# Optimization experiments

Hardware: AMD Instinct MI355X
Metric: run time of the kernel (lower is better)

The kernel has to match this reference:

```python
import jax, jax.numpy as jnp
import numpy as np


def _phi(z, conv_w, conv_b):
    # z: (H, W, S, 1) -> 3x3 SAME conv over state channels -> softmax over states
    x = jnp.transpose(z[..., 0], (2, 0, 1))[None]  # (1, S, H, W)
    y = jax.lax.conv_general_dilated(
        x, conv_w, window_strides=(1, 1), padding='SAME',
        dimension_numbers=('NCHW', 'OIHW', 'NCHW')) + conv_b[None, :, None, None]
    return jax.nn.softmax(jnp.transpose(y[0], (1, 2, 0)), axis=2)[..., None]  # (H, W, S, 1)


def _update(obs, P, u_k, w_k_O, conv_w, conv_b):
    H, W, O = obs.shape
    S = P.shape[0]
    # b = P^T @ obs per cell: b[h,w,s] = sum_o P[o,s] * obs[h,w,o]
    b = jnp.einsum('os,hwo->hws', P, obs)[..., None]  # (H, W, S, 1)
    # Analytic Jacobian db/dP: deriv_b[h,w,s,0,i,j] = obs[h,w,i] * delta(s==j)
    eye = jnp.eye(S, O, dtype=obs.dtype)
    deriv_b = (obs[:, :, None, :, None] * eye[None, None, :, None, :])[:, :, :, None, :, :]  # (H,W,S,1,S,O)

    Bu = b * u_k                                  # (H, W, S, 1)
    bu = jnp.sum(Bu, axis=2, keepdims=True)       # (H, W, 1, 1)
    Z = Bu / bu                                   # Bu / bu

    u_kp1 = _phi(Z, conv_w, conv_b)               # (H, W, S, 1)

    # Sensitivity recursion for obs params (quotient rule on Bu/bu)
    du = deriv_b * u_k[..., None, None] + b[..., None, None] * w_k_O  # (H,W,S,1,S,O)
    term1 = du * bu[..., None, None]
    term2 = jnp.expand_dims(jnp.sum(du, axis=2), 3) * Bu[..., None, None]
    w_pre = (term1 - term2) / bu[..., None, None] ** 2                # (H,W,S,1,S,O)

    # J @ w  ==  9 JVPs of Phi at Z with tangent columns of w (exact, avoids dense (HWS)^2 Jacobian)
    tangents = jnp.moveaxis(w_pre.reshape(H, W, S, 1, S * O), -1, 0)  # (S*O, H, W, S, 1)
    jvp1 = lambda t: jax.jvp(lambda z: _phi(z, conv_w, conv_b), (Z,), (t,))[1]
    w_kp1_O = jnp.moveaxis(jax.vmap(jvp1)(tangents), 0, -1).reshape(H, W, S, 1, S, O)
    return u_kp1, w_kp1_O


def setup_inputs() -> dict:
    key = jax.random.key(0)
    k1, k2, k3 = jax.random.split(key, 3)
    H = W = 512
    S = O = 3
    obs = jax.random.uniform(k1, (H, W, O), dtype=jnp.float32)
    obs_param_matrix = jnp.ones((S, O), jnp.float32) / O          # row-stochastic init
    u_k = jnp.ones((H, W, S, 1), jnp.float32) / S                 # uniform belief
    w_k_O = jnp.zeros((H, W, S, 1, S, O), jnp.float32)
    conv_w = jax.random.normal(k2, (S, S, 3, 3), jnp.float32) * 0.1
    conv_b = jax.random.normal(k3, (S,), jnp.float32) * 0.1
    return {'obs': obs, 'obs_param_matrix': obs_param_matrix, 'u_k': u_k,
            'w_k_O': w_k_O, 'conv_w': conv_w, 'conv_b': conv_b}


def reference(obs, obs_param_matrix, u_k, w_k_O, conv_w, conv_b):
    return _update(obs, obs_param_matrix, u_k, w_k_O, conv_w, conv_b)
```

## Files before the change

kernel.cpp:

```cpp
#include <hip/hip_runtime.h>

#define IMH 512
#define IMW 512
#define TW 32
#define TH 8
#define HW_ (TW + 2)
#define HH_ (TH + 2)
#define NHALO (HW_ * HH_)
#define NTHR 256

__global__ __launch_bounds__(NTHR, 2)
void hmm_fused(const float* __restrict__ obs,
               const float* __restrict__ P,
               const float* __restrict__ u_k,
               const float* __restrict__ w_k,
               const float* __restrict__ conv_w,
               const float* __restrict__ conv_b,
               float* __restrict__ out) {
    __shared__ float4 lds4[NHALO * 8];
    float* lds = (float*)lds4;

    const int tid = threadIdx.x;
    const int w0 = blockIdx.x * TW;
    const int h0 = blockIdx.y * TH;

    float Pm[9];
#pragma unroll
    for (int i = 0; i < 9; ++i) Pm[i] = P[i];

    for (int r = 0; r < HH_; ++r) {
        const int hh = h0 + r - 1;
        if (hh < 0 || hh >= IMH) continue;
        const long long gbase = ((long long)hh * IMW + (w0 - 1)) * 27;
        for (int f = tid; f < HW_ * 27; f += NTHR) {
            const int p = f / 27;
            const int c = f - p * 27;
            const int ww = w0 - 1 + p;
            float v = 0.0f;
            if (ww >= 0 && ww < IMW) v = w_k[gbase + f];
            const int pr = r * HW_ + p;
            lds[pr * 32 + (((c >> 2) + pr) & 7) * 4 + (c & 3)] = v;
        }
    }

    float cw[81];
#pragma unroll
    for (int i = 0; i < 81; ++i) cw[i] = conv_w[i];
    const float cb0 = conv_b[0], cb1 = conv_b[1], cb2 = conv_b[2];

    __syncthreads();

    for (int p = tid; p < NHALO; p += NTHR) {
        const int rr = p / HW_;
        const int cc = p - rr * HW_;
        const int hh = h0 + rr - 1;
        const int ww = w0 + cc - 1;
        float4 o[8];
        if ((unsigned)hh < IMH && (unsigned)ww < IMW) {
            float wv[28];
#pragma unroll
            for (int k = 0; k < 7; ++k) {
                const float4 v = lds4[p * 8 + ((k + p) & 7)];
                wv[4 * k + 0] = v.x; wv[4 * k + 1] = v.y;
                wv[4 * k + 2] = v.z; wv[4 * k + 3] = v.w;
            }
            const int pix = hh * IMW + ww;
            const float ov0 = obs[pix * 3 + 0], ov1 = obs[pix * 3 + 1], ov2 = obs[pix * 3 + 2];
            const float us[3] = {u_k[pix * 3 + 0], u_k[pix * 3 + 1], u_k[pix * 3 + 2]};

            float b[3], Bu[3], bu = 0.0f;
#pragma unroll
            for (int s = 0; s < 3; ++s) {
                b[s] = Pm[0 * 3 + s] * ov0 + Pm[1 * 3 + s] * ov1 + Pm[2 * 3 + s] * ov2;
                Bu[s] = b[s] * us[s];
                bu += Bu[s];
            }
            const float inv_bu = 1.0f / bu;
            float Z[3], oc[32];
#pragma unroll
            for (int s = 0; s < 3; ++s) { Z[s] = Bu[s] * inv_bu; oc[s] = Z[s]; }

            const float ovv[3] = {ov0, ov1, ov2};
#pragma unroll
            for (int i = 0; i < 3; ++i) {
#pragma unroll
                for (int j = 0; j < 3; ++j) {
                    const int ij = i * 3 + j;
                    float du[3], sdu = 0.0f;
#pragma unroll
                    for (int s = 0; s < 3; ++s) {
                        float d = b[s] * wv[s * 9 + ij];
                        if (s == j) d += ovv[i] * us[s];
                        du[s] = d;
                        sdu += d;
                    }
#pragma unroll
                    for (int s = 0; s < 3; ++s)
                        oc[3 + ij * 3 + s] = (du[s] - sdu * Z[s]) * inv_bu;
                }
            }
            oc[30] = 0.0f; oc[31] = 0.0f;
#pragma unroll
            for (int k = 0; k < 8; ++k)
                o[k] = make_float4(oc[4 * k + 0], oc[4 * k + 1], oc[4 * k + 2], oc[4 * k + 3]);
        } else {
#pragma unroll
            for (int k = 0; k < 8; ++k) o[k] = make_float4(0.f, 0.f, 0.f, 0.f);
        }
#pragma unroll
        for (int k = 0; k < 8; ++k) lds4[p * 8 + ((k + p) & 7)] = o[k];
    }

    __syncthreads();

    const int tx = tid & (TW - 1);
    const int ty = tid >> 5;
    const int hp = (ty + 1) * HW_ + tx + 1;

    float acc[30];
#pragma unroll
    for (int i = 0; i < 30; ++i) acc[i] = 0.0f;

#pragma unroll
    for (int ky = 0; ky < 3; ++ky) {
#pragma unroll
        for (int kx = 0; kx < 3; ++kx) {
            const int tap = ky * 3 + kx;
            const int pn = hp + (ky - 1) * HW_ + (kx - 1);
#pragma unroll
            for (int k = 0; k < 8; ++k) {
                const float4 v4 = lds4[pn * 8 + ((k + pn) & 7)];
                const float cv[4] = {v4.x, v4.y, v4.z, v4.w};
#pragma unroll
                for (int j = 0; j < 4; ++j) {
                    const int c = 4 * k + j;
                    if (c < 30) {
                        const int g = c / 3, si = c - (c / 3) * 3;
                        acc[g * 3 + 0] += cw[0 * 27 + si * 9 + tap] * cv[j];
                        acc[g * 3 + 1] += cw[1 * 27 + si * 9 + tap] * cv[j];
                        acc[g * 3 + 2] += cw[2 * 27 + si * 9 + tap] * cv[j];
                    }
                }
            }
        }
    }

    const float y0 = acc[0] + cb0, y1 = acc[1] + cb1, y2 = acc[2] + cb2;
    const float m = fmaxf(y0, fmaxf(y1, y2));
    const float e0 = __expf(y0 - m), e1 = __expf(y1 - m), e2 = __expf(y2 - m);
    const float inv = 1.0f / (e0 + e1 + e2);
    const float p0 = e0 * inv, p1 = e1 * inv, p2 = e2 * inv;

    const int pix = (h0 + ty) * IMW + (w0 + tx);
    out[pix * 3 + 0] = p0; out[pix * 3 + 1] = p1; out[pix * 3 + 2] = p2;

    float wout[27];
#pragma unroll
    for (int g = 1; g < 10; ++g) {
        const float a0 = acc[g * 3 + 0], a1 = acc[g * 3 + 1], a2 = acc[g * 3 + 2];
        const float dot = p0 * a0 + p1 * a1 + p2 * a2;
        const int ij = g - 1;
        wout[0 * 9 + ij] = p0 * (a0 - dot);
        wout[1 * 9 + ij] = p1 * (a1 - dot);
        wout[2 * 9 + ij] = p2 * (a2 - dot);
    }

    __syncthreads();

#pragma unroll
    for (int c = 0; c < 27; ++c) lds[tid * 27 + c] = wout[c];
    __syncthreads();

    float* outw = out + IMH * IMW * 3;
    for (int idx = tid; idx < TW * TH * 27 / 4; idx += NTHR) {
        const int r = idx / 216;
        const int q = idx - r * 216;
        const float4 v = lds4[r * 216 + q];
        float4* dst = (float4*)(outw + ((size_t)(h0 + r) * IMW + w0) * 27);
        dst[q] = v;
    }
}

extern "C" void kernel_launch(void* const* d_in, const int* in_sizes, int n_in,
                              void* d_out, int out_size, void* d_ws, size_t ws_size,
                              hipStream_t stream) {
    const float* obs    = (const float*)d_in[0];
    const float* P      = (const float*)d_in[1];
    const float* u_k    = (const float*)d_in[2];
    const float* w_k    = (const float*)d_in[3];
    const float* conv_w = (const float*)d_in[4];
    const float* conv_b = (const float*)d_in[5];
    float* out = (float*)d_out;

    dim3 grid(IMW / TW, IMH / TH);
    hmm_fused<<<grid, NTHR, 0, stream>>>(obs, P, u_k, w_k, conv_w, conv_b, out);
}
```

Measured before the change: 127.3 us.

## Split sensitivity channels across wave pairs with 512-thread blocks

```diff
diff --git a/kernel.cpp b/kernel.cpp
--- a/kernel.cpp
+++ b/kernel.cpp
@@ -4,12 +4,12 @@
 #define IMW 512
 #define TW 32
 #define TH 8
-#define HW_ (TW + 2)
-#define HH_ (TH + 2)
-#define NHALO (HW_ * HH_)
-#define NTHR 256
-
-__global__ __launch_bounds__(NTHR, 2)
+#define HW_ 34
+#define HH_ 10
+#define NHALO 340
+#define NTHR 512
+
+__global__ __launch_bounds__(NTHR, 1)
 void hmm_fused(const float* __restrict__ obs,
                const float* __restrict__ P,
                const float* __restrict__ u_k,
@@ -20,9 +20,13 @@
     __shared__ float4 lds4[NHALO * 8];
     float* lds = (float*)lds4;
 
-    const int tid = threadIdx.x;
-    const int w0 = blockIdx.x * TW;
-    const int h0 = blockIdx.y * TH;
+    const int tid  = threadIdx.x;
+    const int w0   = blockIdx.x * TW;
+    const int h0   = blockIdx.y * TH;
+    const int lane = tid & 63;
+    const int wave = tid >> 6;
+    const int q    = wave & 1;
+    const int grp  = wave >> 1;
 
     float Pm[9];
 #pragma unroll
@@ -38,8 +42,11 @@
             const int ww = w0 - 1 + p;
             float v = 0.0f;
             if (ww >= 0 && ww < IMW) v = w_k[gbase + f];
+            const int s  = c / 9;
+            const int ij = c - s * 9;
+            const int cd = (ij < 4) ? (3 + ij * 3 + s) : (16 + (ij - 4) * 3 + s);
             const int pr = r * HW_ + p;
-            lds[pr * 32 + (((c >> 2) + pr) & 7) * 4 + (c & 3)] = v;
+            lds[pr * 32 + (((cd >> 2) + pr) & 7) * 4 + (cd & 3)] = v;
         }
     }
 
@@ -50,134 +57,202 @@
 
     __syncthreads();
 
-    for (int p = tid; p < NHALO; p += NTHR) {
+    for (int p = grp * 64 + lane; p < NHALO; p += 256) {
         const int rr = p / HW_;
         const int cc = p - rr * HW_;
         const int hh = h0 + rr - 1;
         const int ww = w0 + cc - 1;
-        float4 o[8];
+        const int base = p * 8;
+        const int kb = q * 4;
+        float oc[16];
         if ((unsigned)hh < IMH && (unsigned)ww < IMW) {
-            float wv[28];
-#pragma unroll
-            for (int k = 0; k < 7; ++k) {
-                const float4 v = lds4[p * 8 + ((k + p) & 7)];
-                wv[4 * k + 0] = v.x; wv[4 * k + 1] = v.y;
-                wv[4 * k + 2] = v.z; wv[4 * k + 3] = v.w;
-            }
             const int pix = hh * IMW + ww;
-            const float ov0 = obs[pix * 3 + 0], ov1 = obs[pix * 3 + 1], ov2 = obs[pix * 3 + 2];
-            const float us[3] = {u_k[pix * 3 + 0], u_k[pix * 3 + 1], u_k[pix * 3 + 2]};
-
-            float b[3], Bu[3], bu = 0.0f;
+            const float ov[3] = {obs[pix*3+0], obs[pix*3+1], obs[pix*3+2]};
+            const float us[3] = {u_k[pix*3+0], u_k[pix*3+1], u_k[pix*3+2]};
+            float b[3], Bu[3], bu = 0.f;
 #pragma unroll
             for (int s = 0; s < 3; ++s) {
-                b[s] = Pm[0 * 3 + s] * ov0 + Pm[1 * 3 + s] * ov1 + Pm[2 * 3 + s] * ov2;
-                Bu[s] = b[s] * us[s];
-                bu += Bu[s];
+                b[s] = Pm[s] * ov[0] + Pm[3+s] * ov[1] + Pm[6+s] * ov[2];
+                Bu[s] = b[s] * us[s]; bu += Bu[s];
             }
             const float inv_bu = 1.0f / bu;
-            float Z[3], oc[32];
-#pragma unroll
-            for (int s = 0; s < 3; ++s) { Z[s] = Bu[s] * inv_bu; oc[s] = Z[s]; }
-
-            const float ovv[3] = {ov0, ov1, ov2};
-#pragma unroll
-            for (int i = 0; i < 3; ++i) {
-#pragma unroll
-                for (int j = 0; j < 3; ++j) {
-                    const int ij = i * 3 + j;
-                    float du[3], sdu = 0.0f;
+            float Z[3];
+#pragma unroll
+            for (int s = 0; s < 3; ++s) Z[s] = Bu[s] * inv_bu;
+
+            float rv[16];
+#pragma unroll
+            for (int k = 0; k < 4; ++k) {
+                const float4 v = lds4[base + ((kb + k + p) & 7)];
+                rv[4*k+0] = v.x; rv[4*k+1] = v.y; rv[4*k+2] = v.z; rv[4*k+3] = v.w;
+            }
+            if (q == 0) {
+                oc[0] = Z[0]; oc[1] = Z[1]; oc[2] = Z[2];
+#pragma unroll
+                for (int ij = 0; ij < 4; ++ij) {
+                    const int i = ij / 3, j = ij % 3;
+                    float du[3], sdu = 0.f;
 #pragma unroll
                     for (int s = 0; s < 3; ++s) {
-                        float d = b[s] * wv[s * 9 + ij];
-                        if (s == j) d += ovv[i] * us[s];
-                        du[s] = d;
-                        sdu += d;
+                        float d = b[s] * rv[3 + ij*3 + s];
+                        if (s == j) d += ov[i] * us[s];
+                        du[s] = d; sdu += d;
                     }
 #pragma unroll
                     for (int s = 0; s < 3; ++s)
-                        oc[3 + ij * 3 + s] = (du[s] - sdu * Z[s]) * inv_bu;
-                }
-            }
-            oc[30] = 0.0f; oc[31] = 0.0f;
-#pragma unroll
-            for (int k = 0; k < 8; ++k)
-                o[k] = make_float4(oc[4 * k + 0], oc[4 * k + 1], oc[4 * k + 2], oc[4 * k + 3]);
+                        oc[3 + ij*3 + s] = (du[s] - sdu * Z[s]) * inv_bu;
+                }
+                oc[15] = 0.f;
+            } else {
+#pragma unroll
+                for (int ij = 4; ij < 9; ++ij) {
+                    const int i = ij / 3, j = ij % 3;
+                    float du[3], sdu = 0.f;
+#pragma unroll
+                    for (int s = 0; s < 3; ++s) {
+                        float d = b[s] * rv[(ij-4)*3 + s];
+                        if (s == j) d += ov[i] * us[s];
+                        du[s] = d; sdu += d;
+                    }
+#pragma unroll
+                    for (int s = 0; s < 3; ++s)
+                        oc[(ij-4)*3 + s] = (du[s] - sdu * Z[s]) * inv_bu;
+                }
+                oc[15] = 0.f;
+            }
         } else {
 #pragma unroll
-            for (int k = 0; k < 8; ++k) o[k] = make_float4(0.f, 0.f, 0.f, 0.f);
-        }
-#pragma unroll
-        for (int k = 0; k < 8; ++k) lds4[p * 8 + ((k + p) & 7)] = o[k];
-    }
-
-    __syncthreads();
-
-    const int tx = tid & (TW - 1);
-    const int ty = tid >> 5;
+            for (int i = 0; i < 16; ++i) oc[i] = 0.f;
+        }
+#pragma unroll
+        for (int k = 0; k < 4; ++k)
+            lds4[base + ((kb + k + p) & 7)] =
+                make_float4(oc[4*k], oc[4*k+1], oc[4*k+2], oc[4*k+3]);
+    }
+
+    __syncthreads();
+
+    const int pxi = grp * 64 + lane;
+    const int tx = pxi & 31, ty = pxi >> 5;
     const int hp = (ty + 1) * HW_ + tx + 1;
 
-    float acc[30];
-#pragma unroll
-    for (int i = 0; i < 30; ++i) acc[i] = 0.0f;
-
-#pragma unroll
-    for (int ky = 0; ky < 3; ++ky) {
-#pragma unroll
-        for (int kx = 0; kx < 3; ++kx) {
-            const int tap = ky * 3 + kx;
-            const int pn = hp + (ky - 1) * HW_ + (kx - 1);
-#pragma unroll
-            for (int k = 0; k < 8; ++k) {
-                const float4 v4 = lds4[pn * 8 + ((k + pn) & 7)];
-                const float cv[4] = {v4.x, v4.y, v4.z, v4.w};
-#pragma unroll
-                for (int j = 0; j < 4; ++j) {
-                    const int c = 4 * k + j;
-                    if (c < 30) {
-                        const int g = c / 3, si = c - (c / 3) * 3;
-                        acc[g * 3 + 0] += cw[0 * 27 + si * 9 + tap] * cv[j];
-                        acc[g * 3 + 1] += cw[1 * 27 + si * 9 + tap] * cv[j];
-                        acc[g * 3 + 2] += cw[2 * 27 + si * 9 + tap] * cv[j];
-                    }
-                }
-            }
-        }
-    }
-
-    const float y0 = acc[0] + cb0, y1 = acc[1] + cb1, y2 = acc[2] + cb2;
-    const float m = fmaxf(y0, fmaxf(y1, y2));
-    const float e0 = __expf(y0 - m), e1 = __expf(y1 - m), e2 = __expf(y2 - m);
+    float yv0 = cb0, yv1 = cb1, yv2 = cb2;
+    float acc[15];
+#pragma unroll
+    for (int i = 0; i < 15; ++i) acc[i] = 0.f;
+
+    if (q == 0) {
+#pragma unroll
+        for (int ky = 0; ky < 3; ++ky) {
+#pragma unroll
+            for (int kx = 0; kx < 3; ++kx) {
+                const int tap = ky * 3 + kx;
+                const int pn = hp + (ky - 1) * HW_ + (kx - 1);
+                float v[16];
+#pragma unroll
+                for (int k = 0; k < 4; ++k) {
+                    const float4 t = lds4[pn*8 + ((k + pn) & 7)];
+                    v[4*k+0] = t.x; v[4*k+1] = t.y; v[4*k+2] = t.z; v[4*k+3] = t.w;
+                }
+#pragma unroll
+                for (int si = 0; si < 3; ++si) {
+                    const float wa = cw[0*27 + si*9 + tap];
+                    const float wb = cw[1*27 + si*9 + tap];
+                    const float wc = cw[2*27 + si*9 + tap];
+                    yv0 += wa * v[si]; yv1 += wb * v[si]; yv2 += wc * v[si];
+#pragma unroll
+                    for (int ij = 0; ij < 4; ++ij) {
+                        const float val = v[3 + ij*3 + si];
+                        acc[ij*3+0] += wa * val;
+                        acc[ij*3+1] += wb * val;
+                        acc[ij*3+2] += wc * val;
+                    }
+                }
+            }
+        }
+    } else {
+#pragma unroll
+        for (int ky = 0; ky < 3; ++ky) {
+#pragma unroll
+            for (int kx = 0; kx < 3; ++kx) {
+                const int tap = ky * 3 + kx;
+                const int pn = hp + (ky - 1) * HW_ + (kx - 1);
+                const float4 t0 = lds4[pn*8 + ((0 + pn) & 7)];
+                const float z[3] = {t0.x, t0.y, t0.z};
+                float v[16];
+#pragma unroll
+                for (int k = 0; k < 4; ++k) {
+                    const float4 t = lds4[pn*8 + ((4 + k + pn) & 7)];
+                    v[4*k+0] = t.x; v[4*k+1] = t.y; v[4*k+2] = t.z; v[4*k+3] = t.w;
+                }
+#pragma unroll
+                for (int si = 0; si < 3; ++si) {
+                    const float wa = cw[0*27 + si*9 + tap];
+                    const float wb = cw[1*27 + si*9 + tap];
+                    const float wc = cw[2*27 + si*9 + tap];
+                    yv0 += wa * z[si]; yv1 += wb * z[si]; yv2 += wc * z[si];
+#pragma unroll
+                    for (int ij = 4; ij < 9; ++ij) {
+                        const float val = v[(ij-4)*3 + si];
+                        acc[(ij-4)*3+0] += wa * val;
+                        acc[(ij-4)*3+1] += wb * val;
+                        acc[(ij-4)*3+2] += wc * val;
+                    }
+                }
+            }
+        }
+    }
+
+    const float m = fmaxf(yv0, fmaxf(yv1, yv2));
+    const float e0 = __expf(yv0 - m), e1 = __expf(yv1 - m), e2 = __expf(yv2 - m);
     const float inv = 1.0f / (e0 + e1 + e2);
     const float p0 = e0 * inv, p1 = e1 * inv, p2 = e2 * inv;
 
-    const int pix = (h0 + ty) * IMW + (w0 + tx);
-    out[pix * 3 + 0] = p0; out[pix * 3 + 1] = p1; out[pix * 3 + 2] = p2;
-
-    float wout[27];
-#pragma unroll
-    for (int g = 1; g < 10; ++g) {
-        const float a0 = acc[g * 3 + 0], a1 = acc[g * 3 + 1], a2 = acc[g * 3 + 2];
-        const float dot = p0 * a0 + p1 * a1 + p2 * a2;
-        const int ij = g - 1;
-        wout[0 * 9 + ij] = p0 * (a0 - dot);
-        wout[1 * 9 + ij] = p1 * (a1 - dot);
-        wout[2 * 9 + ij] = p2 * (a2 - dot);
-    }
-
-    __syncthreads();
-
-#pragma unroll
-    for (int c = 0; c < 27; ++c) lds[tid * 27 + c] = wout[c];
+    float wo[15];
+    const int nij = q ? 5 : 4;
+#pragma unroll
+    for (int ij = 0; ij < 5; ++ij) {
+        if (ij < nij) {
+            const float a0 = acc[ij*3+0], a1 = acc[ij*3+1], a2 = acc[ij*3+2];
+            const float dot = p0*a0 + p1*a1 + p2*a2;
+            wo[ij*3+0] = p0 * (a0 - dot);
+            wo[ij*3+1] = p1 * (a1 - dot);
+            wo[ij*3+2] = p2 * (a2 - dot);
+        }
+    }
+
+    __syncthreads();
+
+    if (q == 0) {
+#pragma unroll
+        for (int ij = 0; ij < 4; ++ij)
+#pragma unroll
+            for (int s = 0; s < 3; ++s)
+                lds[pxi*27 + s*9 + ij] = wo[ij*3+s];
+        lds[6912 + pxi*3 + 0] = p0;
+        lds[6912 + pxi*3 + 1] = p1;
+        lds[6912 + pxi*3 + 2] = p2;
+    } else {
+#pragma unroll
+        for (int ij = 0; ij < 5; ++ij)
+#pragma unroll
+            for (int s = 0; s < 3; ++s)
+                lds[pxi*27 + s*9 + (ij + 4)] = wo[ij*3+s];
+    }
     __syncthreads();
 
     float* outw = out + IMH * IMW * 3;
-    for (int idx = tid; idx < TW * TH * 27 / 4; idx += NTHR) {
+    for (int idx = tid; idx < 1728; idx += NTHR) {
         const int r = idx / 216;
-        const int q = idx - r * 216;
-        const float4 v = lds4[r * 216 + q];
+        const int c4 = idx - r * 216;
         float4* dst = (float4*)(outw + ((size_t)(h0 + r) * IMW + w0) * 27);
-        dst[q] = v;
+        dst[c4] = lds4[idx];
+    }
+    for (int idx = tid; idx < 192; idx += NTHR) {
+        const int r = idx / 24;
+        const int c4 = idx - r * 24;
+        float4* dst = (float4*)(out + ((size_t)(h0 + r) * IMW + w0) * 3);
+        dst[c4] = lds4[1728 + idx];
     }
 }
 
```

Result: slower. 139.2 us (+9.4%).
